# Optimization experiments

Measured on AMD Instinct MI355X. Metric: run time of the kernel, lower is better.

Reference implementation:

```python
import jax, jax.numpy as jnp
import numpy as np

D_MODEL = 192
D_INNER = 384          # expand * d_model
D_STATE = 64
NHEADS = 8             # d_inner / headdim
HEADDIM = 48
D_CONV = 4
CONV_DIM = D_INNER + 2 * D_STATE   # 512 (ngroups=1)
D_IN_PROJ = 2 * D_INNER + 2 * D_STATE + NHEADS  # 904
MIX = 32
EPS = 1e-5


def silu(v):
    return v * jax.nn.sigmoid(v)


def setup_inputs() -> dict:
    key = jax.random.key(0)
    ks = jax.random.split(key, 16)
    B, L, C = 4, 4096, 4
    x = jax.random.normal(ks[0], (B, L, C), jnp.float32)
    Wfc = jax.random.normal(ks[1], (C, D_MODEL), jnp.float32) * 0.3
    bfc = jnp.zeros((D_MODEL,), jnp.float32)
    W_in = jax.random.normal(ks[2], (D_MODEL, D_IN_PROJ), jnp.float32) * 0.02
    conv_w = jax.random.normal(ks[3], (D_CONV, 1, CONV_DIM), jnp.float32) * 0.2  # depthwise (W,I/g,O)
    conv_b = jnp.zeros((CONV_DIM,), jnp.float32)
    # dt_bias = inv_softplus(dt_init) with dt_init ~ U(1e-3, 0.1)
    dt_init = jax.random.uniform(ks[4], (NHEADS,), jnp.float32, 1e-3, 0.1)
    dt_bias = jnp.log(jnp.expm1(dt_init))
    A_log = jnp.log(jax.random.uniform(ks[5], (NHEADS,), jnp.float32, 1.0, 16.0))
    Dparam = jnp.ones((NHEADS,), jnp.float32)
    norm_w = jnp.ones((D_INNER,), jnp.float32)
    W_out = jax.random.normal(ks[6], (D_INNER, D_MODEL), jnp.float32) * 0.02
    W1 = jax.random.normal(ks[7], (D_MODEL, MIX), jnp.float32) * 0.05
    b1 = jnp.zeros((MIX,), jnp.float32)
    W2 = jax.random.normal(ks[8], (MIX, MIX), jnp.float32) * 0.1
    b2 = jnp.zeros((MIX,), jnp.float32)
    Wo = jax.random.normal(ks[9], (MIX, 1), jnp.float32) * 0.1
    bo = jnp.zeros((1,), jnp.float32)
    return {"x": x, "Wfc": Wfc, "bfc": bfc, "W_in": W_in, "conv_w": conv_w,
            "conv_b": conv_b, "dt_bias": dt_bias, "A_log": A_log, "Dparam": Dparam,
            "norm_w": norm_w, "W_out": W_out, "W1": W1, "b1": b1, "W2": W2,
            "b2": b2, "Wo": Wo, "bo": bo}


def _mamba2(h, W_in, conv_w, conv_b, dt_bias, A_log, Dparam, norm_w, W_out):
    B, L, _ = h.shape
    zxbcdt = h @ W_in                                    # (B,L,904)
    z = zxbcdt[..., :D_INNER]
    xBC = zxbcdt[..., D_INNER:D_INNER + CONV_DIM]
    dt = jax.nn.softplus(zxbcdt[..., -NHEADS:] + dt_bias)  # (B,L,H)
    # causal depthwise conv1d
    xBC = jnp.pad(xBC, ((0, 0), (D_CONV - 1, 0), (0, 0)))
    xBC = jax.lax.conv_general_dilated(
        xBC, conv_w, window_strides=(1,), padding="VALID",
        dimension_numbers=("NWC", "WIO", "NWC"), feature_group_count=CONV_DIM)
    xBC = silu(xBC + conv_b)                             # (B,L,512)
    xs = xBC[..., :D_INNER].reshape(B, L, NHEADS, HEADDIM)
    Bm = xBC[..., D_INNER:D_INNER + D_STATE]             # (B,L,N)
    Cm = xBC[..., D_INNER + D_STATE:]                    # (B,L,N)
    A = -jnp.exp(A_log)                                  # (H,)
    dA = jnp.exp(dt * A)                                 # (B,L,H)

    def step(hstate, inp):
        dA_t, dt_t, B_t, x_t, C_t = inp                  # (B,H),(B,H),(B,N),(B,H,P),(B,N)
        dBx_t = jnp.einsum("bh,bn,bhp->bhpn", dt_t, B_t, x_t)
        hstate = dA_t[:, :, None, None] * hstate + dBx_t  # (B,H,P,N)
        y_t = jnp.einsum("bhpn,bn->bhp", hstate, C_t)
        return hstate, y_t

    h0 = jnp.zeros((B, NHEADS, HEADDIM, D_STATE), h.dtype)
    xs_t = jnp.swapaxes(xs, 0, 1)
    _, ys = jax.lax.scan(step, h0, (jnp.swapaxes(dA, 0, 1), jnp.swapaxes(dt, 0, 1),
                                    jnp.swapaxes(Bm, 0, 1), xs_t, jnp.swapaxes(Cm, 0, 1)))
    y = jnp.swapaxes(ys, 0, 1) + Dparam[None, None, :, None] * xs  # (B,L,H,P)
    y = y.reshape(B, L, D_INNER)
    # gated RMSNorm: rmsnorm(y * silu(z)) * weight
    y = y * silu(z)
    y = y * jax.lax.rsqrt(jnp.mean(y * y, axis=-1, keepdims=True) + EPS) * norm_w
    return y @ W_out                                     # (B,L,d_model)


def reference(x, Wfc, bfc, W_in, conv_w, conv_b, dt_bias, A_log, Dparam,
              norm_w, W_out, W1, b1, W2, b2, Wo, bo):
    h = x @ Wfc + bfc                                    # input_fc
    h = _mamba2(h, W_in, conv_w, conv_b, dt_bias, A_log, Dparam, norm_w, W_out)
    m = jax.nn.relu(h @ W1 + b1)
    m = jax.nn.relu(m @ W2 + b2)                         # dropout = identity (eval)
    m = jnp.mean(m, axis=1)                              # pool over time
    angle = (m @ Wo + bo)[:, 0]
    return angle
```

## Files before the change

### kernel.cpp

```cpp
#include <hip/hip_runtime.h>
#include <math.h>


#define BDIM 4
#define LDIM 4096
#define BL (BDIM*LDIM)
#define QC 64
#define NC (LDIM/QC)
#define BH (BDIM*NH)
#define NH 8

#define OFF_W    0u
#define OFF_Z    3145728u
#define OFF_T    9437184u
#define OFF_XS   17825792u
#define OFF_BM   24117248u
#define OFF_CM   25165824u
#define OFF_DT   26214400u
#define OFF_LAC  26345472u
#define OFF_SP   26476544u
#define OFF_Y    32768000u
#define OFF_MACC 39059456u

typedef unsigned short ushort_t;
typedef __attribute__((ext_vector_type(8))) short bf16x8;
typedef __attribute__((ext_vector_type(4))) float f32x4;

__device__ __forceinline__ float sigmoidf_(float x){ return 1.0f/(1.0f+__expf(-x)); }
__device__ __forceinline__ ushort_t f2bf(float x){
  unsigned int u = __float_as_uint(x);
  u += 0x7fffu + ((u>>16)&1u);
  return (ushort_t)(u>>16);
}
__device__ __forceinline__ float bf2f(ushort_t h){
  return __uint_as_float(((unsigned int)h)<<16);
}

__global__ void k_prep(const float* __restrict__ Wfc, const float* __restrict__ bfc,
                       const float* __restrict__ W_in, const float* __restrict__ W_out,
                       const float* __restrict__ W1, const float* __restrict__ norm_w,
                       float* __restrict__ Weff, float* __restrict__ beff,
                       float* __restrict__ Weff2, float* __restrict__ macc,
                       float* __restrict__ ssum){
  int blk = blockIdx.x, tid = threadIdx.x;
  if (blk < 4){
    int n = blk*256 + tid;
    if (n >= 904) return;
    float a0=0.f,a1=0.f,a2=0.f,a3=0.f,ab=0.f;
    for (int d=0; d<192; d++){
      float w = W_in[(size_t)d*904 + n];
      a0 = fmaf(Wfc[d], w, a0);
      a1 = fmaf(Wfc[192+d], w, a1);
      a2 = fmaf(Wfc[384+d], w, a2);
      a3 = fmaf(Wfc[576+d], w, a3);
      ab = fmaf(bfc[d], w, ab);
    }
    Weff[n] = a0; Weff[904+n] = a1; Weff[1808+n] = a2; Weff[2712+n] = a3;
    beff[n] = ab;
  } else if (blk < 52){
    if (blk == 4 && tid < 128) macc[tid] = 0.f;
    int g = (blk-4)*256 + tid;
    int i = g>>5, j = g&31;
    float a = 0.f;
    for (int d=0; d<192; d++) a = fmaf(W_out[(size_t)i*192+d], W1[d*32+j], a);
    Weff2[g] = a * norm_w[i];
  } else {
    int idx = (blk-52)*256 + tid;
    ssum[idx] = 0.f;
  }
}

__global__ __launch_bounds__(256) void k_ipc(
    const float* __restrict__ x, const float* __restrict__ Weff,
    const float* __restrict__ beff, const float* __restrict__ conv_w,
    const float* __restrict__ conv_b, const float* __restrict__ dt_bias,
    ushort_t* __restrict__ xs_h, ushort_t* __restrict__ xs_l,
    ushort_t* __restrict__ Bm_h, ushort_t* __restrict__ Bm_l,
    ushort_t* __restrict__ Cm_h, ushort_t* __restrict__ Cm_l,
    float* __restrict__ dtb){
  __shared__ float sx[7][4];
  int pb = blockIdx.x, tid = threadIdx.x;
  int bl0 = pb*4;
  int l0 = bl0 & 4095, b = bl0 >> 12;
  if (tid < 28){
    int row = tid>>2, r = tid&3;
    int ll = l0-3+row;
    sx[row][r] = (ll>=0) ? x[(size_t)(b*4096+ll)*4 + r] : 0.f;
  }
  __syncthreads();
  if (tid < 32){
    int t = tid>>3, hh = tid&7;
    float raw = beff[896+hh];
    #pragma unroll
    for (int r=0;r<4;r++) raw = fmaf(sx[3+t][r], Weff[r*904+896+hh], raw);
    float xx = raw + dt_bias[hh];
    float dtv = (xx > 20.f) ? xx : log1pf(__expf(xx));
    dtb[(size_t)(b*8+hh)*4096 + l0 + t] = dtv;
  }
  #pragma unroll
  for (int half=0; half<2; half++){
    int c = tid + half*256;
    float w0 = Weff[384+c];
    float w1 = Weff[904+384+c];
    float w2 = Weff[1808+384+c];
    float w3 = Weff[2712+384+c];
    float bb = beff[384+c];
    float cw0 = conv_w[c], cw1 = conv_w[512+c], cw2 = conv_w[1024+c], cw3 = conv_w[1536+c];
    float cb = conv_b[c];
    float pre[7];
    #pragma unroll
    for (int q=0;q<7;q++){
      int ll = l0-3+q;
      float xv = bb;
      xv = fmaf(sx[q][0], w0, xv);
      xv = fmaf(sx[q][1], w1, xv);
      xv = fmaf(sx[q][2], w2, xv);
      xv = fmaf(sx[q][3], w3, xv);
      pre[q] = (ll >= 0) ? xv : 0.f;
    }
    float av[4];
    #pragma unroll
    for (int t=0;t<4;t++){
      float a = cb;
      a = fmaf(cw0,pre[t+0],a); a = fmaf(cw1,pre[t+1],a);
      a = fmaf(cw2,pre[t+2],a); a = fmaf(cw3,pre[t+3],a);
      av[t] = a * sigmoidf_(a);
    }
    if (c < 384){
      int hh = c / 48, p = c - hh*48;
      size_t idx = (size_t)((b*8+hh)*4096 + l0)*48 + p;
      #pragma unroll
      for (int t=0;t<4;t++){
        ushort_t h = f2bf(av[t]);
        xs_h[idx + t*48] = h;
        xs_l[idx + t*48] = f2bf(av[t] - bf2f(h));
      }
    } else if (c < 448){
      size_t idx = (size_t)bl0*64 + (c-384);
      #pragma unroll
      for (int t=0;t<4;t++){
        ushort_t h = f2bf(av[t]);
        Bm_h[idx + t*64] = h;
        Bm_l[idx + t*64] = f2bf(av[t] - bf2f(h));
      }
    } else {
      size_t idx = (size_t)bl0*64 + (c-448);
      #pragma unroll
      for (int t=0;t<4;t++){
        ushort_t h = f2bf(av[t]);
        Cm_h[idx + t*64] = h;
        Cm_l[idx + t*64] = f2bf(av[t] - bf2f(h));
      }
    }
  }
}

__global__ __launch_bounds__(256, 3) void k_phase1(
    const float* __restrict__ dtbuf,
    const ushort_t* __restrict__ Bm_h, const ushort_t* __restrict__ Bm_l,
    const ushort_t* __restrict__ xs_h, const ushort_t* __restrict__ xs_l,
    const float* __restrict__ A_log,
    ushort_t* __restrict__ T, float* __restrict__ lac){
  __shared__ __align__(16) ushort_t sBh[64*72], sBl[64*72];
  __shared__ __align__(16) ushort_t sXh[48*72], sXl[48*72];
  __shared__ float sdt[64], sla[64], sw[64];
  int tid = threadIdx.x, blk = blockIdx.x;
  int bh = blk >> 6, k = blk & 63;
  int b = bh >> 3, hh = bh & 7;
  int t0 = k*64;
  int w = tid>>6, lane = tid&63, l15 = lane&15, quad = lane>>4;

  if (tid < 64) sdt[tid] = dtbuf[(size_t)bh*4096 + t0 + tid];
  __syncthreads();
  if (tid == 0){
    float eA = __expf(A_log[hh]);
    float cum = 0.f;
    for (int i=0;i<64;i++){ cum -= sdt[i]*eA; sla[i] = cum; }
  }
  __syncthreads();
  if (tid < 64){
    sw[tid] = __expf(sla[63]-sla[tid])*sdt[tid];
    lac[(size_t)blk*64 + tid] = sla[tid];
  }
  __syncthreads();
  {
    int s2 = (tid&31)*2, ng = (tid>>5)*8;
    size_t base0 = (size_t)(b*4096+t0+s2)*64 + ng;
    ushort_t h0a[8], l0a[8], h1a[8], l1a[8];
    *(uint4*)h0a = *(const uint4*)(Bm_h + base0);
    *(uint4*)l0a = *(const uint4*)(Bm_l + base0);
    *(uint4*)h1a = *(const uint4*)(Bm_h + base0 + 64);
    *(uint4*)l1a = *(const uint4*)(Bm_l + base0 + 64);
    float w0 = sw[s2], w1 = sw[s2+1];
    #pragma unroll
    for (int c=0;c<8;c++){
      float f0 = (bf2f(h0a[c]) + bf2f(l0a[c])) * w0;
      float f1 = (bf2f(h1a[c]) + bf2f(l1a[c])) * w1;
      ushort_t h0 = f2bf(f0), h1 = f2bf(f1);
      ushort_t lo0 = f2bf(f0-bf2f(h0)), lo1 = f2bf(f1-bf2f(h1));
      int o = (ng+c)*72 + s2;
      *(unsigned int*)&sBh[o] = (unsigned int)h0 | ((unsigned int)h1<<16);
      *(unsigned int*)&sBl[o] = (unsigned int)lo0 | ((unsigned int)lo1<<16);
    }
  }
  {
    int s2 = (tid>>3)*2, p0 = (tid&7)*6;
    const ushort_t* xh0 = xs_h + (size_t)(bh*4096+t0+s2)*48 + p0;
    const ushort_t* xl0 = xs_l + (size_t)(bh*4096+t0+s2)*48 + p0;
    #pragma unroll
    for (int c=0;c<6;c++){
      unsigned int hv = (unsigned int)xh0[c] | ((unsigned int)xh0[48+c]<<16);
      unsigned int lv = (unsigned int)xl0[c] | ((unsigned int)xl0[48+c]<<16);
      int o = (p0+c)*72 + s2;
      *(unsigned int*)&sXh[o] = hv;
      *(unsigned int*)&sXl[o] = lv;
    }
  }
  __syncthreads();
  f32x4 acc[3];
  #pragma unroll
  for (int t=0;t<3;t++) acc[t] = (f32x4)(0.f);
  #pragma unroll
  for (int ks=0;ks<2;ks++){
    int bo = (w*16+l15)*72 + ks*32 + quad*8;
    bf16x8 bbh = *(bf16x8*)&sBh[bo];
    bf16x8 bbl = *(bf16x8*)&sBl[bo];
    #pragma unroll
    for (int pt=0;pt<3;pt++){
      int xo = (pt*16+l15)*72 + ks*32 + quad*8;
      bf16x8 xah = *(bf16x8*)&sXh[xo];
      bf16x8 xal = *(bf16x8*)&sXl[xo];
      acc[pt] = __builtin_amdgcn_mfma_f32_16x16x32_bf16(xah, bbh, acc[pt], 0,0,0);
      acc[pt] = __builtin_amdgcn_mfma_f32_16x16x32_bf16(xah, bbl, acc[pt], 0,0,0);
      acc[pt] = __builtin_amdgcn_mfma_f32_16x16x32_bf16(xal, bbh, acc[pt], 0,0,0);
    }
  }
  {
    ushort_t* dst = T + (size_t)blk*3072;
    #pragma unroll
    for (int pt=0;pt<3;pt++)
      #pragma unroll
      for (int r=0;r<4;r++)
        dst[(pt*16+quad*4+r)*64 + w*16 + l15] = f2bf(acc[pt][r]);
  }
}

__global__ __launch_bounds__(256) void k_phase2p(
    const ushort_t* __restrict__ T, const float* __restrict__ lac,
    ushort_t* __restrict__ Sp){
  __shared__ __align__(16) float sT[64*64];
  __shared__ __align__(16) float sW[64][68];
  __shared__ float sc[64];
  int tid = threadIdx.x;
  int bh = blockIdx.x, es = blockIdx.y;
  #pragma unroll
  for (int r=0;r<2;r++){
    int idx = tid + r*256;
    int row = idx>>3, g8 = (idx&7)*8;
    ushort_t tv[8];
    *(uint4*)tv = *(const uint4*)(T + (size_t)(bh*64+row)*3072 + es*64 + g8);
    #pragma unroll
    for (int c=0;c<8;c++) sT[row*64 + g8 + c] = bf2f(tv[c]);
  }
  if (tid < 64) sc[tid] = __expf(lac[(size_t)(bh*64+tid)*64 + 63]);
  __syncthreads();
  if (tid < 64){
    int k = tid;
    float w = 1.f;
    for (int j=63; j>=0; --j){
      bool a = (j < k);
      sW[j][k] = a ? w : 0.f;
      if (a) w *= sc[j];
    }
  }
  __syncthreads();
  int k0 = (tid>>4)*4, e0 = (tid&15)*4;
  float acc[4][4];
  #pragma unroll
  for (int i=0;i<4;i++)
    #pragma unroll
    for (int j=0;j<4;j++) acc[i][j]=0.f;
  int jmax = k0+2; if (jmax > 62) jmax = 62;
  for (int j=0; j<=jmax; ++j){
    float wv[4], tv[4];
    *(float4*)wv = *(float4*)&sW[j][k0];
    *(float4*)tv = *(float4*)&sT[j*64 + e0];
    #pragma unroll
    for (int i=0;i<4;i++)
      #pragma unroll
      for (int e=0;e<4;e++) acc[i][e] = fmaf(wv[i], tv[e], acc[i][e]);
  }
  #pragma unroll
  for (int i=0;i<4;i++){
    ushort4 h4;
    ushort_t* hp = (ushort_t*)&h4;
    #pragma unroll
    for (int e=0;e<4;e++) hp[e] = f2bf(acc[i][e]);
    *(ushort4*)(Sp + (size_t)(bh*64+k0+i)*3072 + es*64 + e0) = h4;
  }
}

__global__ __launch_bounds__(256, 3) void k_phase3(
    const float* __restrict__ dtbuf, const float* __restrict__ lac,
    const ushort_t* __restrict__ Bm_h, const ushort_t* __restrict__ Bm_l,
    const ushort_t* __restrict__ Cm_h, const ushort_t* __restrict__ Cm_l,
    const ushort_t* __restrict__ xs_h, const ushort_t* __restrict__ xs_l,
    const ushort_t* __restrict__ Sp, const float* __restrict__ Dparam,
    const float* __restrict__ xg, const float* __restrict__ Weff,
    const float* __restrict__ beff,
    ushort_t* __restrict__ g16, float* __restrict__ ssum){
  __shared__ __align__(16) ushort_t sCh[64*72], sCl[64*72];
  __shared__ __align__(16) ushort_t sBh[64*72], sBl[64*72];
  __shared__ __align__(16) ushort_t sXh[48*72], sXl[48*72];
  __shared__ float sla[64], sdt[64];
  int tid = threadIdx.x, blk = blockIdx.x;
  int bh = blk>>6, k = blk&63, b = bh>>3, hh = bh&7, t0 = k*64;
  int w = tid>>6, lane = tid&63, l15 = lane&15, quad = lane>>4;

  if (tid < 64){
    sdt[tid] = dtbuf[(size_t)bh*4096 + t0 + tid];
    sla[tid] = lac[(size_t)blk*64 + tid];
  }
  {
    int row = tid>>2, ng = (tid&3)*16;
    size_t gb = (size_t)(b*4096+t0+row)*64 + ng;
    int o = row*72 + ng;
    *(uint4*)&sCh[o]   = *(const uint4*)(Cm_h + gb);
    *(uint4*)&sCh[o+8] = *(const uint4*)(Cm_h + gb + 8);
    *(uint4*)&sCl[o]   = *(const uint4*)(Cm_l + gb);
    *(uint4*)&sCl[o+8] = *(const uint4*)(Cm_l + gb + 8);
    *(uint4*)&sBh[o]   = *(const uint4*)(Bm_h + gb);
    *(uint4*)&sBh[o+8] = *(const uint4*)(Bm_h + gb + 8);
    *(uint4*)&sBl[o]   = *(const uint4*)(Bm_l + gb);
    *(uint4*)&sBl[o+8] = *(const uint4*)(Bm_l + gb + 8);
  }
  {
    int s2 = (tid>>3)*2, p0 = (tid&7)*6;
    const ushort_t* xh0 = xs_h + (size_t)(bh*4096+t0+s2)*48 + p0;
    const ushort_t* xl0 = xs_l + (size_t)(bh*4096+t0+s2)*48 + p0;
    #pragma unroll
    for (int c=0;c<6;c++){
      unsigned int hv = (unsigned int)xh0[c] | ((unsigned int)xh0[48+c]<<16);
      unsigned int lv = (unsigned int)xl0[c] | ((unsigned int)xl0[48+c]<<16);
      int o = (p0+c)*72 + s2;
      *(unsigned int*)&sXh[o] = hv;
      *(unsigned int*)&sXl[o] = lv;
    }
  }
  __syncthreads();

  f32x4 gacc[4];
  #pragma unroll
  for (int t=0;t<4;t++) gacc[t] = (f32x4)(0.f);
  {
    bf16x8 cah[2], cal[2];
    #pragma unroll
    for (int ks=0;ks<2;ks++){
      int ao = (w*16+l15)*72 + ks*32 + quad*8;
      cah[ks] = *(bf16x8*)&sCh[ao];
      cal[ks] = *(bf16x8*)&sCl[ao];
    }
    for (int bs=0; bs<=w; ++bs){
      #pragma unroll
      for (int ks=0;ks<2;ks++){
        int bo = (bs*16+l15)*72 + ks*32 + quad*8;
        bf16x8 bhf = *(bf16x8*)&sBh[bo];
        bf16x8 blf = *(bf16x8*)&sBl[bo];
        gacc[bs] = __builtin_amdgcn_mfma_f32_16x16x32_bf16(cah[ks], bhf, gacc[bs], 0,0,0);
        gacc[bs] = __builtin_amdgcn_mfma_f32_16x16x32_bf16(cah[ks], blf, gacc[bs], 0,0,0);
        gacc[bs] = __builtin_amdgcn_mfma_f32_16x16x32_bf16(cal[ks], bhf, gacc[bs], 0,0,0);
      }
    }
  }
  __syncthreads();

  for (int bs=0; bs<=w; ++bs){
    #pragma unroll
    for (int r=0;r<4;r++){
      int i = w*16 + quad*4 + r;
      int s = bs*16 + l15;
      float v = 0.f;
      if (s <= i) v = gacc[bs][r] * __expf(sla[i]-sla[s]) * sdt[s];
      sBh[i*72+s] = f2bf(v);
    }
  }
  if (w==0){
    #pragma unroll
    for (int r=0;r<4;r++) sBh[(quad*4+r)*72 + 16+l15] = 0;
  }
  if (w==2){
    #pragma unroll
    for (int r=0;r<4;r++) sBh[(32+quad*4+r)*72 + 48+l15] = 0;
  }
  __syncthreads();

  bf16x8 pah[3][2];
  {
    const ushort_t* sph = Sp + (size_t)blk*3072;
    #pragma unroll
    for (int pt=0;pt<3;pt++)
      #pragma unroll
      for (int ks=0;ks<2;ks++)
        pah[pt][ks] = *(const bf16x8*)(sph + (size_t)(pt*16+l15)*64 + ks*32 + quad*8);
  }

  f32x4 accI[3], accA[3];
  #pragma unroll
  for (int t=0;t<3;t++){ accI[t] = (f32x4)(0.f); accA[t] = (f32x4)(0.f); }
  int nks = (w>=2) ? 2 : 1;
  for (int ks=0; ks<nks; ++ks){
    int go = (w*16+l15)*72 + ks*32 + quad*8;
    bf16x8 gbh = *(bf16x8*)&sBh[go];
    #pragma unroll
    for (int pt=0;pt<3;pt++){
      int xo = (pt*16+l15)*72 + ks*32 + quad*8;
      bf16x8 xah = *(bf16x8*)&sXh[xo];
      bf16x8 xal = *(bf16x8*)&sXl[xo];
      accI[pt] = __builtin_amdgcn_mfma_f32_16x16x32_bf16(xah, gbh, accI[pt], 0,0,0);
      accI[pt] = __builtin_amdgcn_mfma_f32_16x16x32_bf16(xal, gbh, accI[pt], 0,0,0);
    }
  }
  #pragma unroll
  for (int ks=0; ks<2; ++ks){
    int co = (w*16+l15)*72 + ks*32 + quad*8;
    bf16x8 cbh = *(bf16x8*)&sCh[co];
    bf16x8 cbl = *(bf16x8*)&sCl[co];
    #pragma unroll
    for (int pt=0;pt<3;pt++){
      accA[pt] = __builtin_amdgcn_mfma_f32_16x16x32_bf16(pah[pt][ks], cbh, accA[pt], 0,0,0);
      accA[pt] = __builtin_amdgcn_mfma_f32_16x16x32_bf16(pah[pt][ks], cbl, accA[pt], 0,0,0);
    }
  }
  {
    int i = w*16 + l15;
    int tok = b*4096 + t0 + i;
    float eli = __expf(sla[i]);
    float Dh = Dparam[hh];
    float4 xv = *(const float4*)(xg + (size_t)tok*4);
    ushort_t* gbase = g16 + (size_t)tok*384 + hh*48;
    float ssq = 0.f;
    #pragma unroll
    for (int pt=0;pt<3;pt++)
      #pragma unroll
      for (int r=0;r<4;r++){
        int p = pt*16 + quad*4 + r;
        float xf = bf2f(sXh[p*72 + i]) + bf2f(sXl[p*72 + i]);
        float yv = accI[pt][r] + eli*accA[pt][r] + Dh*xf;
        int e = hh*48 + p;
        float zv = beff[e];
        zv = fmaf(xv.x, Weff[e], zv);
        zv = fmaf(xv.y, Weff[904+e], zv);
        zv = fmaf(xv.z, Weff[1808+e], zv);
        zv = fmaf(xv.w, Weff[2712+e], zv);
        float gg = yv * (zv * sigmoidf_(zv));
        gbase[p] = f2bf(gg);
        ssq += gg*gg;
      }
    ssq += __shfl_xor(ssq, 16);
    ssq += __shfl_xor(ssq, 32);
    if (quad == 0) atomicAdd(&ssum[tok], ssq);
  }
}

__global__ __launch_bounds__(256) void k_mlp2(
    const ushort_t* __restrict__ g16, const float* __restrict__ ssum,
    const float* __restrict__ Weff2, const float* __restrict__ b1,
    const float* __restrict__ W2, const float* __restrict__ b2,
    float* __restrict__ macc){
  __shared__ __align__(16) float sW[384][32];
  __shared__ __align__(16) float sm1[64][33];
  __shared__ __align__(16) float sW2[32][32];
  __shared__ __align__(16) float sm2[64][33];
  int tid = threadIdx.x;
  int tok0 = blockIdx.x*64;
  int b = tok0 >> 12;
  #pragma unroll
  for (int r=0;r<12;r++){
    int idx = tid + r*256;
    int row = idx>>3, c4 = (idx&7)*4;
    *(float4*)&sW[row][c4] = *(const float4*)(Weff2 + (size_t)idx*4);
  }
  {
    int row = tid>>3, c4 = (tid&7)*4;
    *(float4*)&sW2[row][c4] = *(const float4*)(W2 + row*32 + c4);
  }
  __syncthreads();
  {
    int tk = tid>>3, j0 = (tid&7)*4;
    float rms0 = rsqrtf(ssum[tok0+tk]*(1.f/384.f) + 1e-5f);
    float rms1 = rsqrtf(ssum[tok0+tk+32]*(1.f/384.f) + 1e-5f);
    float a0[4], a1[4];
    #pragma unroll
    for (int j=0;j<4;j++){ a0[j] = b1[j0+j]; a1[j] = a0[j]; }
    const ushort_t* y0 = g16 + (size_t)(tok0+tk)*384;
    const ushort_t* y1 = g16 + (size_t)(tok0+tk+32)*384;
    for (int k8=0;k8<48;k8++){
      ushort_t ua[8], ub[8];
      *(uint4*)ua = *(const uint4*)(y0 + k8*8);
      *(uint4*)ub = *(const uint4*)(y1 + k8*8);
      #pragma unroll
      for (int c=0;c<8;c++){
        float va = bf2f(ua[c])*rms0, vb = bf2f(ub[c])*rms1;
        float w[4]; *(float4*)w = *(float4*)&sW[k8*8+c][j0];
        #pragma unroll
        for (int j=0;j<4;j++){ a0[j] = fmaf(va, w[j], a0[j]); a1[j] = fmaf(vb, w[j], a1[j]); }
      }
    }
    #pragma unroll
    for (int j=0;j<4;j++){
      sm1[tk][j0+j]    = fmaxf(a0[j], 0.f);
      sm1[tk+32][j0+j] = fmaxf(a1[j], 0.f);
    }
  }
  __syncthreads();
  {
    int tk = tid>>3, j0 = (tid&7)*4;
    float a0[4], a1[4];
    #pragma unroll
    for (int j=0;j<4;j++){ a0[j] = b2[j0+j]; a1[j] = a0[j]; }
    #pragma unroll
    for (int kk=0;kk<32;kk++){
      float va = sm1[tk][kk];
      float vb = sm1[tk+32][kk];
      float w[4]; *(float4*)w = *(float4*)&sW2[kk][j0];
      #pragma unroll
      for (int j=0;j<4;j++){ a0[j] = fmaf(va, w[j], a0[j]); a1[j] = fmaf(vb, w[j], a1[j]); }
    }
    #pragma unroll
    for (int j=0;j<4;j++){
      sm2[tk][j0+j]    = fmaxf(a0[j], 0.f);
      sm2[tk+32][j0+j] = fmaxf(a1[j], 0.f);
    }
  }
  __syncthreads();
  if (tid < 32){
    float t = 0.f;
    #pragma unroll
    for (int tok=0;tok<64;tok++) t += sm2[tok][tid];
    atomicAdd(&macc[b*32 + tid], t);
  }
}

__global__ void k_final(const float* __restrict__ macc, const float* __restrict__ Wo,
                        const float* __restrict__ bo, float* __restrict__ out){
  int tid = threadIdx.x;
  if (tid < 4){
    float acc = bo[0];
    #pragma unroll
    for (int j=0;j<32;j++) acc = fmaf(macc[tid*32+j]*(1.f/4096.f), Wo[j], acc);
    out[tid] = acc;
  }
}

extern "C" void kernel_launch(void* const* d_in, const int* in_sizes, int n_in,
                              void* d_out, int out_size, void* d_ws, size_t ws_size,
                              hipStream_t stream){
  const float* x      = (const float*)d_in[0];
  const float* Wfc    = (const float*)d_in[1];
  const float* bfc    = (const float*)d_in[2];
  const float* W_in   = (const float*)d_in[3];
  const float* conv_w = (const float*)d_in[4];
  const float* conv_b = (const float*)d_in[5];
  const float* dt_bias= (const float*)d_in[6];
  const float* A_log  = (const float*)d_in[7];
  const float* Dparam = (const float*)d_in[8];
  const float* norm_w = (const float*)d_in[9];
  const float* W_out  = (const float*)d_in[10];
  const float* W1     = (const float*)d_in[11];
  const float* b1     = (const float*)d_in[12];
  const float* W2     = (const float*)d_in[13];
  const float* b2     = (const float*)d_in[14];
  const float* Wo     = (const float*)d_in[15];
  const float* bo     = (const float*)d_in[16];
  float* ws  = (float*)d_ws;
  float* out = (float*)d_out;

  float* Weff  = ws + OFF_W;
  float* beff  = ws + OFF_W + 4096;
  float* Weff2 = ws + OFF_W + 8192;
  float* ssum  = ws + OFF_Z;
  ushort_t* Tb   = (ushort_t*)(ws + OFF_T);
  ushort_t* xs_h = (ushort_t*)(ws + OFF_XS);
  ushort_t* xs_l = xs_h + 6291456u;
  ushort_t* Bm_h = (ushort_t*)(ws + OFF_BM);
  ushort_t* Bm_l = Bm_h + 1048576u;
  ushort_t* Cm_h = (ushort_t*)(ws + OFF_CM);
  ushort_t* Cm_l = Cm_h + 1048576u;
  float* dtb   = ws + OFF_DT;
  float* lacb  = ws + OFF_LAC;
  ushort_t* Spb  = (ushort_t*)(ws + OFF_SP);
  ushort_t* g16 = (ushort_t*)(ws + OFF_Y);
  float* macc  = ws + OFF_MACC;

  k_prep<<<dim3(116), dim3(256), 0, stream>>>(Wfc, bfc, W_in, W_out, W1, norm_w,
                                              Weff, beff, Weff2, macc, ssum);
  k_ipc<<<dim3(BL/4), dim3(256), 0, stream>>>(x, Weff, beff, conv_w, conv_b,
                                              dt_bias, xs_h, xs_l, Bm_h, Bm_l,
                                              Cm_h, Cm_l, dtb);
  k_phase1<<<dim3(BH*NC), dim3(256), 0, stream>>>(dtb, Bm_h, Bm_l, xs_h, xs_l,
                                                  A_log, Tb, lacb);
  k_phase2p<<<dim3(BH,48), dim3(256), 0, stream>>>(Tb, lacb, Spb);
  k_phase3<<<dim3(BH*NC), dim3(256), 0, stream>>>(dtb, lacb, Bm_h, Bm_l,
                                                  Cm_h, Cm_l, xs_h, xs_l,
                                                  Spb, Dparam, x, Weff, beff,
                                                  g16, ssum);
  k_mlp2<<<dim3(BL/64), dim3(256), 0, stream>>>(g16, ssum, Weff2, b1, W2, b2, macc);
  k_final<<<dim3(1), dim3(64), 0, stream>>>(macc, Wo, bo, out);
}
```

Baseline: 186.1 us.

## Drop bf16 hi/lo split for xs and B in phase1, fuse final into mlp2

Stores xs as a single bf16 value instead of a hi/lo pair. In phase1 it also drops the low part of the scaled B operand. Phase3 drops the low parts of xs and C in its matrix products. This halves the MFMA count and the shared/global traffic for those operands, at some cost in accuracy. Separately, the k_final launch is folded into k_mlp2 using an atomic counter, so the last block computes the output and one kernel launch is removed.

Result: slower. 193.4 us (+3.9%).

```diff
diff --git a/kernel.cpp b/kernel.cpp
--- a/kernel.cpp
+++ b/kernel.cpp
@@ -41,7 +41,7 @@
                        const float* __restrict__ W1, const float* __restrict__ norm_w,
                        float* __restrict__ Weff, float* __restrict__ beff,
                        float* __restrict__ Weff2, float* __restrict__ macc,
-                       float* __restrict__ ssum){
+                       float* __restrict__ ssum, unsigned int* __restrict__ cnt){
   int blk = blockIdx.x, tid = threadIdx.x;
   if (blk < 4){
     int n = blk*256 + tid;
@@ -59,6 +59,7 @@
     beff[n] = ab;
   } else if (blk < 52){
     if (blk == 4 && tid < 128) macc[tid] = 0.f;
+    if (blk == 5 && tid == 0) *cnt = 0u;
     int g = (blk-4)*256 + tid;
     int i = g>>5, j = g&31;
     float a = 0.f;
@@ -74,7 +75,7 @@
     const float* __restrict__ x, const float* __restrict__ Weff,
     const float* __restrict__ beff, const float* __restrict__ conv_w,
     const float* __restrict__ conv_b, const float* __restrict__ dt_bias,
-    ushort_t* __restrict__ xs_h, ushort_t* __restrict__ xs_l,
+    ushort_t* __restrict__ xs,
     ushort_t* __restrict__ Bm_h, ushort_t* __restrict__ Bm_l,
     ushort_t* __restrict__ Cm_h, ushort_t* __restrict__ Cm_l,
     float* __restrict__ dtb){
@@ -130,11 +131,7 @@
       int hh = c / 48, p = c - hh*48;
       size_t idx = (size_t)((b*8+hh)*4096 + l0)*48 + p;
       #pragma unroll
-      for (int t=0;t<4;t++){
-        ushort_t h = f2bf(av[t]);
-        xs_h[idx + t*48] = h;
-        xs_l[idx + t*48] = f2bf(av[t] - bf2f(h));
-      }
+      for (int t=0;t<4;t++) xs[idx + t*48] = f2bf(av[t]);
     } else if (c < 448){
       size_t idx = (size_t)bl0*64 + (c-384);
       #pragma unroll
@@ -157,12 +154,12 @@
 
 __global__ __launch_bounds__(256, 3) void k_phase1(
     const float* __restrict__ dtbuf,
-    const ushort_t* __restrict__ Bm_h, const ushort_t* __restrict__ Bm_l,
-    const ushort_t* __restrict__ xs_h, const ushort_t* __restrict__ xs_l,
+    const ushort_t* __restrict__ Bm_h,
+    const ushort_t* __restrict__ xs,
     const float* __restrict__ A_log,
     ushort_t* __restrict__ T, float* __restrict__ lac){
-  __shared__ __align__(16) ushort_t sBh[64*72], sBl[64*72];
-  __shared__ __align__(16) ushort_t sXh[48*72], sXl[48*72];
+  __shared__ __align__(16) ushort_t sBs[64*72];
+  __shared__ __align__(16) ushort_t sXs[48*72];
   __shared__ float sdt[64], sla[64], sw[64];
   int tid = threadIdx.x, blk = blockIdx.x;
   int bh = blk >> 6, k = blk & 63;
@@ -186,34 +183,24 @@
   {
     int s2 = (tid&31)*2, ng = (tid>>5)*8;
     size_t base0 = (size_t)(b*4096+t0+s2)*64 + ng;
-    ushort_t h0a[8], l0a[8], h1a[8], l1a[8];
+    ushort_t h0a[8], h1a[8];
     *(uint4*)h0a = *(const uint4*)(Bm_h + base0);
-    *(uint4*)l0a = *(const uint4*)(Bm_l + base0);
     *(uint4*)h1a = *(const uint4*)(Bm_h + base0 + 64);
-    *(uint4*)l1a = *(const uint4*)(Bm_l + base0 + 64);
     float w0 = sw[s2], w1 = sw[s2+1];
     #pragma unroll
     for (int c=0;c<8;c++){
-      float f0 = (bf2f(h0a[c]) + bf2f(l0a[c])) * w0;
-      float f1 = (bf2f(h1a[c]) + bf2f(l1a[c])) * w1;
-      ushort_t h0 = f2bf(f0), h1 = f2bf(f1);
-      ushort_t lo0 = f2bf(f0-bf2f(h0)), lo1 = f2bf(f1-bf2f(h1));
-      int o = (ng+c)*72 + s2;
-      *(unsigned int*)&sBh[o] = (unsigned int)h0 | ((unsigned int)h1<<16);
-      *(unsigned int*)&sBl[o] = (unsigned int)lo0 | ((unsigned int)lo1<<16);
+      ushort_t h0 = f2bf(bf2f(h0a[c]) * w0);
+      ushort_t h1 = f2bf(bf2f(h1a[c]) * w1);
+      *(unsigned int*)&sBs[(ng+c)*72 + s2] = (unsigned int)h0 | ((unsigned int)h1<<16);
     }
   }
   {
     int s2 = (tid>>3)*2, p0 = (tid&7)*6;
-    const ushort_t* xh0 = xs_h + (size_t)(bh*4096+t0+s2)*48 + p0;
-    const ushort_t* xl0 = xs_l + (size_t)(bh*4096+t0+s2)*48 + p0;
+    const ushort_t* xh0 = xs + (size_t)(bh*4096+t0+s2)*48 + p0;
     #pragma unroll
     for (int c=0;c<6;c++){
       unsigned int hv = (unsigned int)xh0[c] | ((unsigned int)xh0[48+c]<<16);
-      unsigned int lv = (unsigned int)xl0[c] | ((unsigned int)xl0[48+c]<<16);
-      int o = (p0+c)*72 + s2;
-      *(unsigned int*)&sXh[o] = hv;
-      *(unsigned int*)&sXl[o] = lv;
+      *(unsigned int*)&sXs[(p0+c)*72 + s2] = hv;
     }
   }
   __syncthreads();
@@ -223,16 +210,12 @@
   #pragma unroll
   for (int ks=0;ks<2;ks++){
     int bo = (w*16+l15)*72 + ks*32 + quad*8;
-    bf16x8 bbh = *(bf16x8*)&sBh[bo];
-    bf16x8 bbl = *(bf16x8*)&sBl[bo];
+    bf16x8 bbs = *(bf16x8*)&sBs[bo];
     #pragma unroll
     for (int pt=0;pt<3;pt++){
       int xo = (pt*16+l15)*72 + ks*32 + quad*8;
-      bf16x8 xah = *(bf16x8*)&sXh[xo];
-      bf16x8 xal = *(bf16x8*)&sXl[xo];
-      acc[pt] = __builtin_amdgcn_mfma_f32_16x16x32_bf16(xah, bbh, acc[pt], 0,0,0);
-      acc[pt] = __builtin_amdgcn_mfma_f32_16x16x32_bf16(xah, bbl, acc[pt], 0,0,0);
-      acc[pt] = __builtin_amdgcn_mfma_f32_16x16x32_bf16(xal, bbh, acc[pt], 0,0,0);
+      bf16x8 xas = *(bf16x8*)&sXs[xo];
+      acc[pt] = __builtin_amdgcn_mfma_f32_16x16x32_bf16(xas, bbs, acc[pt], 0,0,0);
     }
   }
   {
@@ -304,14 +287,14 @@
     const float* __restrict__ dtbuf, const float* __restrict__ lac,
     const ushort_t* __restrict__ Bm_h, const ushort_t* __restrict__ Bm_l,
     const ushort_t* __restrict__ Cm_h, const ushort_t* __restrict__ Cm_l,
-    const ushort_t* __restrict__ xs_h, const ushort_t* __restrict__ xs_l,
+    const ushort_t* __restrict__ xs,
     const ushort_t* __restrict__ Sp, const float* __restrict__ Dparam,
     const float* __restrict__ xg, const float* __restrict__ Weff,
     const float* __restrict__ beff,
     ushort_t* __restrict__ g16, float* __restrict__ ssum){
   __shared__ __align__(16) ushort_t sCh[64*72], sCl[64*72];
   __shared__ __align__(16) ushort_t sBh[64*72], sBl[64*72];
-  __shared__ __align__(16) ushort_t sXh[48*72], sXl[48*72];
+  __shared__ __align__(16) ushort_t sXs[48*72];
   __shared__ float sla[64], sdt[64];
   int tid = threadIdx.x, blk = blockIdx.x;
   int bh = blk>>6, k = blk&63, b = bh>>3, hh = bh&7, t0 = k*64;
@@ -336,15 +319,11 @@
   }
   {
     int s2 = (tid>>3)*2, p0 = (tid&7)*6;
-    const ushort_t* xh0 = xs_h + (size_t)(bh*4096+t0+s2)*48 + p0;
-    const ushort_t* xl0 = xs_l + (size_t)(bh*4096+t0+s2)*48 + p0;
+    const ushort_t* xh0 = xs + (size_t)(bh*4096+t0+s2)*48 + p0;
     #pragma unroll
     for (int c=0;c<6;c++){
       unsigned int hv = (unsigned int)xh0[c] | ((unsigned int)xh0[48+c]<<16);
-      unsigned int lv = (unsigned int)xl0[c] | ((unsigned int)xl0[48+c]<<16);
-      int o = (p0+c)*72 + s2;
-      *(unsigned int*)&sXh[o] = hv;
-      *(unsigned int*)&sXl[o] = lv;
+      *(unsigned int*)&sXs[(p0+c)*72 + s2] = hv;
     }
   }
   __syncthreads();
@@ -413,23 +392,17 @@
     bf16x8 gbh = *(bf16x8*)&sBh[go];
     #pragma unroll
     for (int pt=0;pt<3;pt++){
-      int xo = (pt*16+l15)*72 + ks*32 + quad*8;
-      bf16x8 xah = *(bf16x8*)&sXh[xo];
-      bf16x8 xal = *(bf16x8*)&sXl[xo];
-      accI[pt] = __builtin_amdgcn_mfma_f32_16x16x32_bf16(xah, gbh, accI[pt], 0,0,0);
-      accI[pt] = __builtin_amdgcn_mfma_f32_16x16x32_bf16(xal, gbh, accI[pt], 0,0,0);
+      bf16x8 xas = *(bf16x8*)&sXs[(pt*16+l15)*72 + ks*32 + quad*8];
+      accI[pt] = __builtin_amdgcn_mfma_f32_16x16x32_bf16(xas, gbh, accI[pt], 0,0,0);
     }
   }
   #pragma unroll
   for (int ks=0; ks<2; ++ks){
     int co = (w*16+l15)*72 + ks*32 + quad*8;
     bf16x8 cbh = *(bf16x8*)&sCh[co];
-    bf16x8 cbl = *(bf16x8*)&sCl[co];
-    #pragma unroll
-    for (int pt=0;pt<3;pt++){
+    #pragma unroll
+    for (int pt=0;pt<3;pt++)
       accA[pt] = __builtin_amdgcn_mfma_f32_16x16x32_bf16(pah[pt][ks], cbh, accA[pt], 0,0,0);
-      accA[pt] = __builtin_amdgcn_mfma_f32_16x16x32_bf16(pah[pt][ks], cbl, accA[pt], 0,0,0);
-    }
   }
   {
     int i = w*16 + l15;
@@ -444,7 +417,7 @@
       #pragma unroll
       for (int r=0;r<4;r++){
         int p = pt*16 + quad*4 + r;
-        float xf = bf2f(sXh[p*72 + i]) + bf2f(sXl[p*72 + i]);
+        float xf = bf2f(sXs[p*72 + i]);
         float yv = accI[pt][r] + eli*accA[pt][r] + Dh*xf;
         int e = hh*48 + p;
         float zv = beff[e];
@@ -466,11 +439,14 @@
     const ushort_t* __restrict__ g16, const float* __restrict__ ssum,
     const float* __restrict__ Weff2, const float* __restrict__ b1,
     const float* __restrict__ W2, const float* __restrict__ b2,
-    float* __restrict__ macc){
+    float* __restrict__ macc, unsigned int* __restrict__ cnt,
+    const float* __restrict__ Wo, const float* __restrict__ bo,
+    float* __restrict__ out){
   __shared__ __align__(16) float sW[384][32];
   __shared__ __align__(16) float sm1[64][33];
   __shared__ __align__(16) float sW2[32][32];
   __shared__ __align__(16) float sm2[64][33];
+  __shared__ int slast;
   int tid = threadIdx.x;
   int tok0 = blockIdx.x*64;
   int b = tok0 >> 12;
@@ -539,16 +515,21 @@
     for (int tok=0;tok<64;tok++) t += sm2[tok][tid];
     atomicAdd(&macc[b*32 + tid], t);
   }
-}
-
-__global__ void k_final(const float* __restrict__ macc, const float* __restrict__ Wo,
-                        const float* __restrict__ bo, float* __restrict__ out){
-  int tid = threadIdx.x;
-  if (tid < 4){
-    float acc = bo[0];
-    #pragma unroll
-    for (int j=0;j<32;j++) acc = fmaf(macc[tid*32+j]*(1.f/4096.f), Wo[j], acc);
-    out[tid] = acc;
+  __threadfence();
+  __syncthreads();
+  if (tid == 0){
+    unsigned int old = atomicAdd(cnt, 1u);
+    slast = (old == (unsigned int)(gridDim.x - 1)) ? 1 : 0;
+  }
+  __syncthreads();
+  if (slast){
+    __threadfence();
+    if (tid < 4){
+      float acc = bo[0];
+      #pragma unroll
+      for (int j=0;j<32;j++) acc = fmaf(macc[tid*32+j]*(1.f/4096.f), Wo[j], acc);
+      out[tid] = acc;
+    }
   }
 }
 
@@ -580,8 +561,7 @@
   float* Weff2 = ws + OFF_W + 8192;
   float* ssum  = ws + OFF_Z;
   ushort_t* Tb   = (ushort_t*)(ws + OFF_T);
-  ushort_t* xs_h = (ushort_t*)(ws + OFF_XS);
-  ushort_t* xs_l = xs_h + 6291456u;
+  ushort_t* xsb  = (ushort_t*)(ws + OFF_XS);
   ushort_t* Bm_h = (ushort_t*)(ws + OFF_BM);
   ushort_t* Bm_l = Bm_h + 1048576u;
   ushort_t* Cm_h = (ushort_t*)(ws + OFF_CM);
@@ -591,19 +571,19 @@
   ushort_t* Spb  = (ushort_t*)(ws + OFF_SP);
   ushort_t* g16 = (ushort_t*)(ws + OFF_Y);
   float* macc  = ws + OFF_MACC;
+  unsigned int* cnt = (unsigned int*)(ws + OFF_MACC + 128);
 
   k_prep<<<dim3(116), dim3(256), 0, stream>>>(Wfc, bfc, W_in, W_out, W1, norm_w,
-                                              Weff, beff, Weff2, macc, ssum);
+                                              Weff, beff, Weff2, macc, ssum, cnt);
   k_ipc<<<dim3(BL/4), dim3(256), 0, stream>>>(x, Weff, beff, conv_w, conv_b,
-                                              dt_bias, xs_h, xs_l, Bm_h, Bm_l,
+                                              dt_bias, xsb, Bm_h, Bm_l,
                                               Cm_h, Cm_l, dtb);
-  k_phase1<<<dim3(BH*NC), dim3(256), 0, stream>>>(dtb, Bm_h, Bm_l, xs_h, xs_l,
-                                                  A_log, Tb, lacb);
+  k_phase1<<<dim3(BH*NC), dim3(256), 0, stream>>>(dtb, Bm_h, xsb, A_log, Tb, lacb);
   k_phase2p<<<dim3(BH,48), dim3(256), 0, stream>>>(Tb, lacb, Spb);
   k_phase3<<<dim3(BH*NC), dim3(256), 0, stream>>>(dtb, lacb, Bm_h, Bm_l,
-                                                  Cm_h, Cm_l, xs_h, xs_l,
+                                                  Cm_h, Cm_l, xsb,
                                                   Spb, Dparam, x, Weff, beff,
                                                   g16, ssum);
-  k_mlp2<<<dim3(BL/64), dim3(256), 0, stream>>>(g16, ssum, Weff2, b1, W2, b2, macc);
-  k_final<<<dim3(1), dim3(64), 0, stream>>>(macc, Wo, bo, out);
-}
+  k_mlp2<<<dim3(BL/64), dim3(256), 0, stream>>>(g16, ssum, Weff2, b1, W2, b2,
+                                                macc, cnt, Wo, bo, out);
+}
```
